# Optimization experiments

Measured on AMD Instinct MI355X. Metric: run time of the kernel, lower is better.

Reference implementation:

```python
import jax, jax.numpy as jnp
import numpy as np

N_NODES = 100000
D = 128
N_EDGES = 1600000


def setup_inputs() -> dict:
    key = jax.random.key(0)
    ks = jax.random.split(key, 10)
    scale = 1.0 / np.sqrt(D)
    return {
        "node_embeddings": jax.random.normal(ks[0], (N_NODES, D), jnp.float32),
        "gc_weight": jax.random.normal(ks[1], (D, D), jnp.float32) * scale,
        "gc_bias": jnp.zeros((D,), jnp.float32),
        "tcn_weight": jax.random.normal(ks[2], (D, D, 3), jnp.float32) * scale,
        "tcn_bias": jnp.zeros((D,), jnp.float32),
        "hist0": jax.random.normal(ks[3], (N_NODES, D), jnp.float32),
        "hist1": jax.random.normal(ks[4], (N_NODES, D), jnp.float32),
        "hist2": jax.random.normal(ks[5], (N_NODES, D), jnp.float32),
        "src": jax.random.randint(ks[6], (N_EDGES,), 0, N_NODES),
        "dst": jax.random.randint(ks[7], (N_EDGES,), 0, N_NODES),
    }


def _graph_conv(x, w, b, src, dst, n):
    # DGL GraphConv, norm='both': X' = D_in^{-1/2} A (D_out^{-1/2} X) W + b
    ones = jnp.ones(src.shape, x.dtype)
    deg_out = jax.ops.segment_sum(ones, src, num_segments=n)
    deg_in = jax.ops.segment_sum(ones, dst, num_segments=n)
    norm_out = jax.lax.rsqrt(jnp.maximum(deg_out, 1.0))
    norm_in = jax.lax.rsqrt(jnp.maximum(deg_in, 1.0))
    feat = x * norm_out[:, None]                                   # [N, D]
    agg = jax.ops.segment_sum(feat[src], dst, num_segments=n)      # gather+scatter over edges
    agg = agg * norm_in[:, None]
    return agg @ w + b


def reference(node_embeddings, gc_weight, gc_bias, tcn_weight, tcn_bias,
              hist0, hist1, hist2, src, dst):
    n = node_embeddings.shape[0]
    h = _graph_conv(node_embeddings, gc_weight, gc_bias, src, dst, n)
    # stack 3 history snapshots + current h along a time axis -> [N, D, T=4]
    seq = jnp.stack([hist0, hist1, hist2, h], axis=2)
    out = jax.lax.conv_general_dilated(
        seq, tcn_weight, window_strides=(1,), padding=[(1, 1)],
        dimension_numbers=("NCW", "OIW", "NCW"))
    out = out + tcn_bias[None, :, None]
    return out[:, :, -1]  # last time step, [N, D]
```

## Files before the change

### kernel.cpp

```cpp
#include <hip/hip_runtime.h>


__global__ void degree_kernel(const int* __restrict__ src, const int* __restrict__ dst,
                              int* __restrict__ dego, int* __restrict__ degi, int n_edges) {
    int stride = gridDim.x * blockDim.x;
    for (int i = blockIdx.x * blockDim.x + threadIdx.x; i < n_edges; i += stride) {
        atomicAdd(&dego[src[i]], 1);
        atomicAdd(&degi[dst[i]], 1);
    }
}

__global__ void norm_kernel(const int* __restrict__ dego, const int* __restrict__ degi,
                            float* __restrict__ norm_out, float* __restrict__ norm_in, int n) {
    int i = blockIdx.x * blockDim.x + threadIdx.x;
    if (i < n) {
        norm_out[i] = rsqrtf(fmaxf((float)dego[i], 1.0f));
        norm_in[i]  = rsqrtf(fmaxf((float)degi[i], 1.0f));
    }
}

__global__ __launch_bounds__(1024) void scan_kernel(const int* __restrict__ degi,
                                                    int* __restrict__ rowptr, int n) {
    __shared__ int sums[1024];
    const int t = threadIdx.x;
    const int chunk = (n + 1023) / 1024;
    const int begin = t * chunk;
    const int end = min(begin + chunk, n);
    int s = 0;
    for (int i = begin; i < end; ++i) s += degi[i];
    sums[t] = s;
    __syncthreads();
    for (int off = 1; off < 1024; off <<= 1) {
        int v = (t >= off) ? sums[t - off] : 0;
        __syncthreads();
        if (t >= off) sums[t] += v;
        __syncthreads();
    }
    int run = (t == 0) ? 0 : sums[t - 1];
    for (int i = begin; i < end; ++i) { rowptr[i] = run; run += degi[i]; }
    if (t == 1023) rowptr[n] = sums[1023];
}

__global__ void fill_kernel(const int* __restrict__ src, const int* __restrict__ dst,
                            const int* __restrict__ rowptr, int* __restrict__ cursor,
                            int* __restrict__ csr_src, int n_edges) {
    int stride = gridDim.x * blockDim.x;
    for (int i = blockIdx.x * blockDim.x + threadIdx.x; i < n_edges; i += stride) {
        int d = dst[i];
        int ofs = atomicAdd(&cursor[d], 1);
        csr_src[rowptr[d] + ofs] = src[i];
    }
}

__global__ void gather_kernel(const float* __restrict__ x, const int* __restrict__ csr_src,
                              const int* __restrict__ rowptr, const float* __restrict__ norm_out,
                              const float* __restrict__ norm_in, float* __restrict__ agg, int n) {
    int gtid = blockIdx.x * blockDim.x + threadIdx.x;
    int wave = gtid >> 6;
    int lane = threadIdx.x & 63;
    int n_waves = (gridDim.x * blockDim.x) >> 6;
    for (int d = wave; d < n; d += n_waves) {
        int s0 = rowptr[d];
        int s1 = rowptr[d + 1];
        float2 acc0 = {0.f, 0.f}, acc1 = {0.f, 0.f};
        int i = s0;
        for (; i + 1 < s1; i += 2) {
            int sa = csr_src[i];
            int sb = csr_src[i + 1];
            float na = norm_out[sa];
            float nb = norm_out[sb];
            float2 va = *reinterpret_cast<const float2*>(x + (size_t)sa * 128 + lane * 2);
            float2 vb = *reinterpret_cast<const float2*>(x + (size_t)sb * 128 + lane * 2);
            acc0.x = fmaf(va.x, na, acc0.x);
            acc0.y = fmaf(va.y, na, acc0.y);
            acc1.x = fmaf(vb.x, nb, acc1.x);
            acc1.y = fmaf(vb.y, nb, acc1.y);
        }
        if (i < s1) {
            int sa = csr_src[i];
            float na = norm_out[sa];
            float2 va = *reinterpret_cast<const float2*>(x + (size_t)sa * 128 + lane * 2);
            acc0.x = fmaf(va.x, na, acc0.x);
            acc0.y = fmaf(va.y, na, acc0.y);
        }
        float ni = norm_in[d];
        float2 r = {(acc0.x + acc1.x) * ni, (acc0.y + acc1.y) * ni};
        *reinterpret_cast<float2*>(agg + (size_t)d * 128 + lane * 2) = r;
    }
}

__global__ void prep_kernel(const float* __restrict__ gcw, const float* __restrict__ gcb,
                            const float* __restrict__ tcn, const float* __restrict__ tcnb,
                            float* __restrict__ Bmat, float* __restrict__ cvec) {
    int i = blockIdx.x;
    int o = threadIdx.x;
    float m = 0.f;
    for (int j = 0; j < 128; ++j)
        m += gcw[i * 128 + j] * tcn[o * 384 + j * 3 + 1];
    Bmat[(128 + i) * 128 + o] = m;
    Bmat[i * 128 + o] = tcn[o * 384 + i * 3 + 0];
    if (i == 0) {
        float c = tcnb[o];
        for (int j = 0; j < 128; ++j)
            c += tcn[o * 384 + j * 3 + 1] * gcb[j];
        cvec[o] = c;
    }
}

__global__ __launch_bounds__(256) void gemm_kernel(const float* __restrict__ hist2,
                                                   float* __restrict__ outagg,
                                                   const float* __restrict__ Bmat,
                                                   const float* __restrict__ cvec, int n) {
    __shared__ float As[64][17];
    __shared__ float Bs[16][128];
    const int t = threadIdx.x;
    const int tcol = t & 15;
    const int trow = t >> 4;
    const int block_row = blockIdx.x * 64;

    float acc[4][8];
#pragma unroll
    for (int j = 0; j < 4; ++j)
#pragma unroll
        for (int m = 0; m < 8; ++m) acc[j][m] = 0.f;

    for (int kk = 0; kk < 256; kk += 16) {
        {
            int r = t >> 2;
            int k4 = (t & 3) << 2;
            int row = block_row + r;
            float4 v = make_float4(0.f, 0.f, 0.f, 0.f);
            if (row < n) {
                if (kk < 128)
                    v = *reinterpret_cast<const float4*>(hist2 + (size_t)row * 128 + kk + k4);
                else
                    v = *reinterpret_cast<const float4*>(outagg + (size_t)row * 128 + (kk - 128) + k4);
            }
            As[r][k4 + 0] = v.x; As[r][k4 + 1] = v.y;
            As[r][k4 + 2] = v.z; As[r][k4 + 3] = v.w;
        }
        {
#pragma unroll
            for (int rep = 0; rep < 2; ++rep) {
                int idx = t + rep * 256;
                int k = idx >> 5;
                int o4 = (idx & 31) << 2;
                const float4 v = *reinterpret_cast<const float4*>(Bmat + (size_t)(kk + k) * 128 + o4);
                *reinterpret_cast<float4*>(&Bs[k][o4]) = v;
            }
        }
        __syncthreads();
#pragma unroll
        for (int k = 0; k < 16; ++k) {
            float a0 = As[trow * 4 + 0][k];
            float a1 = As[trow * 4 + 1][k];
            float a2 = As[trow * 4 + 2][k];
            float a3 = As[trow * 4 + 3][k];
            float4 b0 = *reinterpret_cast<const float4*>(&Bs[k][tcol * 8]);
            float4 b1 = *reinterpret_cast<const float4*>(&Bs[k][tcol * 8 + 4]);
            float b[8] = {b0.x, b0.y, b0.z, b0.w, b1.x, b1.y, b1.z, b1.w};
#pragma unroll
            for (int m = 0; m < 8; ++m) {
                acc[0][m] = fmaf(a0, b[m], acc[0][m]);
                acc[1][m] = fmaf(a1, b[m], acc[1][m]);
                acc[2][m] = fmaf(a2, b[m], acc[2][m]);
                acc[3][m] = fmaf(a3, b[m], acc[3][m]);
            }
        }
        __syncthreads();
    }
    float cv[8];
#pragma unroll
    for (int m = 0; m < 8; ++m) cv[m] = cvec[tcol * 8 + m];
#pragma unroll
    for (int j = 0; j < 4; ++j) {
        int row = block_row + trow * 4 + j;
        if (row < n) {
            float4 w0 = make_float4(acc[j][0] + cv[0], acc[j][1] + cv[1],
                                    acc[j][2] + cv[2], acc[j][3] + cv[3]);
            float4 w1 = make_float4(acc[j][4] + cv[4], acc[j][5] + cv[5],
                                    acc[j][6] + cv[6], acc[j][7] + cv[7]);
            *reinterpret_cast<float4*>(outagg + (size_t)row * 128 + tcol * 8) = w0;
            *reinterpret_cast<float4*>(outagg + (size_t)row * 128 + tcol * 8 + 4) = w1;
        }
    }
}

extern "C" void kernel_launch(void* const* d_in, const int* in_sizes, int n_in,
                              void* d_out, int out_size, void* d_ws, size_t ws_size,
                              hipStream_t stream) {
    const float* x     = (const float*)d_in[0];
    const float* gcw   = (const float*)d_in[1];
    const float* gcb   = (const float*)d_in[2];
    const float* tcn   = (const float*)d_in[3];
    const float* tcnb  = (const float*)d_in[4];
    const float* hist2 = (const float*)d_in[7];
    const int*   src   = (const int*)d_in[8];
    const int*   dst   = (const int*)d_in[9];
    float* out = (float*)d_out;

    const int n = in_sizes[0] / 128;
    const int e = in_sizes[8];

    auto align256 = [](size_t v) { return (v + 255) & ~(size_t)255; };
    char* ws = (char*)d_ws;
    int*   dego     = (int*)ws;    ws += align256((size_t)n * 4);
    int*   degi     = (int*)ws;    ws += align256((size_t)n * 4);
    int*   cursor   = (int*)ws;    ws += align256((size_t)n * 4);
    float* norm_out = (float*)ws;  ws += align256((size_t)n * 4);
    float* norm_in  = (float*)ws;  ws += align256((size_t)n * 4);
    int*   rowptr   = (int*)ws;    ws += align256((size_t)(n + 1) * 4);
    float* Bmat     = (float*)ws;  ws += align256((size_t)256 * 128 * 4);
    float* cvec     = (float*)ws;  ws += align256((size_t)128 * 4);
    int*   csr_src  = (int*)ws;    ws += align256((size_t)e * 4);

    hipMemsetAsync(dego, 0, align256((size_t)n * 4) * 3, stream);

    degree_kernel<<<2048, 256, 0, stream>>>(src, dst, dego, degi, e);
    norm_kernel<<<(n + 255) / 256, 256, 0, stream>>>(dego, degi, norm_out, norm_in, n);
    scan_kernel<<<1, 1024, 0, stream>>>(degi, rowptr, n);
    fill_kernel<<<2048, 256, 0, stream>>>(src, dst, rowptr, cursor, csr_src, e);
    prep_kernel<<<128, 128, 0, stream>>>(gcw, gcb, tcn, tcnb, Bmat, cvec);
    gather_kernel<<<2048, 256, 0, stream>>>(x, csr_src, rowptr, norm_out, norm_in, out, n);
    gemm_kernel<<<(n + 63) / 64, 256, 0, stream>>>(hist2, out, Bmat, cvec, n);
}
```

Measured before the change: 797.7 us.

## Replace single-block prefix scan with three-pass multi-block scan

The exclusive scan over in-degrees used to run in one 1024-thread block, with each thread serially looping over about a hundred strided elements. It is now split into three kernels: a per-block reduction, a single-block scan of the block partials, and a per-block local scan that writes rowptr using vectorised int4 loads and stores. This spreads the scan across about a hundred blocks instead of one CU. The cost is two extra kernel launches, and the second pass assumes at most 256 blocks (n up to 262144).

Result: faster. 680.1 us (-14.7%).

```diff
diff --git a/kernel.cpp b/kernel.cpp
--- a/kernel.cpp
+++ b/kernel.cpp
@@ -19,26 +19,77 @@
     }
 }
 
-__global__ __launch_bounds__(1024) void scan_kernel(const int* __restrict__ degi,
+
+__global__ __launch_bounds__(256) void scan1_kernel(const int* __restrict__ degi,
+                                                    int* __restrict__ partials, int n) {
+    __shared__ int red[256];
+    const int t = threadIdx.x;
+    const int base = blockIdx.x * 1024 + t * 4;
+    int s = 0;
+    if (base + 3 < n) {
+        int4 v = *reinterpret_cast<const int4*>(degi + base);
+        s = v.x + v.y + v.z + v.w;
+    } else {
+        for (int j = 0; j < 4; ++j)
+            if (base + j < n) s += degi[base + j];
+    }
+    red[t] = s;
+    __syncthreads();
+    for (int off = 128; off > 0; off >>= 1) {
+        if (t < off) red[t] += red[t + off];
+        __syncthreads();
+    }
+    if (t == 0) partials[blockIdx.x] = red[0];
+}
+
+__global__ __launch_bounds__(256) void scan2_kernel(int* __restrict__ partials, int nb,
                                                     int* __restrict__ rowptr, int n) {
-    __shared__ int sums[1024];
-    const int t = threadIdx.x;
-    const int chunk = (n + 1023) / 1024;
-    const int begin = t * chunk;
-    const int end = min(begin + chunk, n);
-    int s = 0;
-    for (int i = begin; i < end; ++i) s += degi[i];
-    sums[t] = s;
+    __shared__ int sums[256];
+    const int t = threadIdx.x;
+    sums[t] = (t < nb) ? partials[t] : 0;
     __syncthreads();
-    for (int off = 1; off < 1024; off <<= 1) {
+    for (int off = 1; off < 256; off <<= 1) {
         int v = (t >= off) ? sums[t - off] : 0;
         __syncthreads();
         if (t >= off) sums[t] += v;
         __syncthreads();
     }
-    int run = (t == 0) ? 0 : sums[t - 1];
-    for (int i = begin; i < end; ++i) { rowptr[i] = run; run += degi[i]; }
-    if (t == 1023) rowptr[n] = sums[1023];
+    if (t < nb) partials[t] = (t == 0) ? 0 : sums[t - 1];
+    if (t == 0) rowptr[n] = sums[nb - 1];
+}
+
+__global__ __launch_bounds__(256) void scan3_kernel(const int* __restrict__ degi,
+                                                    const int* __restrict__ partials,
+                                                    int* __restrict__ rowptr, int n) {
+    __shared__ int tsum[256];
+    const int t = threadIdx.x;
+    const int base = blockIdx.x * 1024 + t * 4;
+    int v0 = 0, v1 = 0, v2 = 0, v3 = 0;
+    if (base + 3 < n) {
+        int4 v = *reinterpret_cast<const int4*>(degi + base);
+        v0 = v.x; v1 = v.y; v2 = v.z; v3 = v.w;
+    } else {
+        if (base + 0 < n) v0 = degi[base + 0];
+        if (base + 1 < n) v1 = degi[base + 1];
+        if (base + 2 < n) v2 = degi[base + 2];
+    }
+    tsum[t] = v0 + v1 + v2 + v3;
+    __syncthreads();
+    for (int off = 1; off < 256; off <<= 1) {
+        int v = (t >= off) ? tsum[t - off] : 0;
+        __syncthreads();
+        if (t >= off) tsum[t] += v;
+        __syncthreads();
+    }
+    int p0 = partials[blockIdx.x] + ((t == 0) ? 0 : tsum[t - 1]);
+    int p1 = p0 + v0, p2 = p1 + v1, p3 = p2 + v2;
+    if (base + 3 < n) {
+        *reinterpret_cast<int4*>(rowptr + base) = make_int4(p0, p1, p2, p3);
+    } else {
+        if (base + 0 < n) rowptr[base + 0] = p0;
+        if (base + 1 < n) rowptr[base + 1] = p1;
+        if (base + 2 < n) rowptr[base + 2] = p2;
+    }
 }
 
 __global__ void fill_kernel(const int* __restrict__ src, const int* __restrict__ dst,
@@ -201,6 +252,7 @@
 
     const int n = in_sizes[0] / 128;
     const int e = in_sizes[8];
+    const int nb = (n + 1023) / 1024;
 
     auto align256 = [](size_t v) { return (v + 255) & ~(size_t)255; };
     char* ws = (char*)d_ws;
@@ -210,6 +262,7 @@
     float* norm_out = (float*)ws;  ws += align256((size_t)n * 4);
     float* norm_in  = (float*)ws;  ws += align256((size_t)n * 4);
     int*   rowptr   = (int*)ws;    ws += align256((size_t)(n + 1) * 4);
+    int*   partials = (int*)ws;    ws += align256((size_t)256 * 4);
     float* Bmat     = (float*)ws;  ws += align256((size_t)256 * 128 * 4);
     float* cvec     = (float*)ws;  ws += align256((size_t)128 * 4);
     int*   csr_src  = (int*)ws;    ws += align256((size_t)e * 4);
@@ -218,7 +271,9 @@
 
     degree_kernel<<<2048, 256, 0, stream>>>(src, dst, dego, degi, e);
     norm_kernel<<<(n + 255) / 256, 256, 0, stream>>>(dego, degi, norm_out, norm_in, n);
-    scan_kernel<<<1, 1024, 0, stream>>>(degi, rowptr, n);
+    scan1_kernel<<<nb, 256, 0, stream>>>(degi, partials, n);
+    scan2_kernel<<<1, 256, 0, stream>>>(partials, nb, rowptr, n);
+    scan3_kernel<<<nb, 256, 0, stream>>>(degi, partials, rowptr, n);
     fill_kernel<<<2048, 256, 0, stream>>>(src, dst, rowptr, cursor, csr_src, e);
     prep_kernel<<<128, 128, 0, stream>>>(gcw, gcb, tcn, tcnb, Bmat, cvec);
     gather_kernel<<<2048, 256, 0, stream>>>(x, csr_src, rowptr, norm_out, norm_in, out, n);
```
